# Performance work log

Measured on AMD Instinct MI355X. Metric: run time of the kernel, lower is better.

## Reference

```python
import jax, jax.numpy as jnp
import numpy as np

N = 100000   # num_nodes
E = 1600000  # num_edges (avg degree 16)
IN = 128     # input_dim
H = 4        # num_heads
D = 32       # hidden_dim per head (H*D == 128)
NEG_SLOPE = 0.2


def setup_inputs() -> dict:
    key = jax.random.key(0)
    ks = jax.random.split(key, 8)
    s = 0.1
    x = jax.random.normal(ks[0], (N, IN), jnp.float32)
    edge_index = jax.random.randint(ks[1], (2, E), 0, N, dtype=jnp.int32)
    W_gat = jax.random.normal(ks[2], (H * D, IN), jnp.float32) * s   # GATConv lin weight
    att_src = jax.random.normal(ks[3], (H, D), jnp.float32) * s
    att_dst = jax.random.normal(ks[4], (H, D), jnp.float32) * s
    bias_gat = jnp.zeros((H * D,), jnp.float32)
    W_lin = jax.random.normal(ks[5], (IN, H * D), jnp.float32) * s   # nn.Linear weight
    b_lin = jnp.zeros((IN,), jnp.float32)
    return {"x": x, "edge_index": edge_index, "W_gat": W_gat,
            "att_src": att_src, "att_dst": att_dst, "bias_gat": bias_gat,
            "W_lin": W_lin, "b_lin": b_lin}


def reference(x, edge_index, W_gat, att_src, att_dst, bias_gat, W_lin, b_lin):
    # (eval mode: all dropouts are identity; sparse edge weights unused in original)
    h = (x @ W_gat.T).reshape(N, H, D)                 # [N,H,D] per-head projections
    a_s = jnp.einsum('nhd,hd->nh', h, att_src)         # [N,H]
    a_d = jnp.einsum('nhd,hd->nh', h, att_dst)         # [N,H]
    # add self loops (PyG default)
    loop = jnp.arange(N, dtype=edge_index.dtype)
    src = jnp.concatenate([edge_index[0], loop])       # [E+N]
    dst = jnp.concatenate([edge_index[1], loop])       # [E+N]
    logits = jax.nn.leaky_relu(a_s[src] + a_d[dst], NEG_SLOPE)  # [E+N,H]
    # segment softmax over edges grouped by destination node
    m = jax.ops.segment_max(logits, dst, num_segments=N)        # [N,H]
    e = jnp.exp(logits - m[dst])
    denom = jax.ops.segment_sum(e, dst, num_segments=N)         # [N,H]
    alpha = e / denom[dst]                                      # [E+N,H]
    # scatter-aggregate weighted source features
    agg = jax.ops.segment_sum(alpha[:, :, None] * h[src], dst, num_segments=N)
    out = agg.reshape(N, H * D) + bias_gat             # concat heads + bias
    out = jax.nn.relu(out)
    return out @ W_lin.T + b_lin                       # [N, IN]
```

## Files before the change

### kernel.cpp

```cpp
#include <hip/hip_runtime.h>
#include <hip/hip_bf16.h>
#include <hip/hip_fp16.h>

#define NN 100000
#define EE 1600000
#define INF_DIM 128
#define NHEAD 4
#define HDIM 32
#define NEG_SLOPE 0.2f

typedef __attribute__((ext_vector_type(8))) short short8;
typedef __attribute__((ext_vector_type(4))) float floatx4;

__device__ __forceinline__ unsigned short f2bf(float x) {
  union { float f; unsigned int u; } c;
  c.f = x;
  const unsigned int r = c.u + 0x7fffu + ((c.u >> 16) & 1u);
  return (unsigned short)(r >> 16);
}
__device__ __forceinline__ unsigned int cvtpk_bf16(float lo, float hi) {
  unsigned int r;
  asm("v_cvt_pk_bf16_f32 %0, %1, %2" : "=v"(r) : "v"(lo), "v"(hi));
  return r;
}
__device__ __forceinline__ unsigned int packh2(float a, float b) {
  const __half ha = __float2half(a), hb = __float2half(b);
  const unsigned short ua = *(const unsigned short*)&ha;
  const unsigned short ub = *(const unsigned short*)&hb;
  return (unsigned int)ua | ((unsigned int)ub << 16);
}
__device__ __forceinline__ float pickw(const int4 e, const int head) {
  const unsigned int d = (head & 2) ? (unsigned int)e.z : (unsigned int)e.y;
  const unsigned short us =
      (head & 1) ? (unsigned short)(d >> 16) : (unsigned short)(d & 0xffffu);
  const __half h = *(const __half*)&us;
  return __half2float(h);
}
__device__ __forceinline__ void accum8h(const uint4 g, const float c,
                                        float* acc) {
  union { uint4 u; __half2 h[4]; } v;
  v.u = g;
#pragma unroll
  for (int j = 0; j < 4; ++j) {
    const float2 f = __half22float2(v.h[j]);
    acc[2 * j] = fmaf(c, f.x, acc[2 * j]);
    acc[2 * j + 1] = fmaf(c, f.y, acc[2 * j + 1]);
  }
}

#define LDA 136

__global__ __launch_bounds__(256) void gemm_mfma(
    const float* __restrict__ Af, const unsigned short* __restrict__ Ab,
    const unsigned short* __restrict__ W16, const float* __restrict__ bias,
    unsigned short* __restrict__ Ch, float* __restrict__ Cf,
    const float* __restrict__ att_src, const float* __restrict__ att_dst,
    float* __restrict__ a_s, float* __restrict__ a_d, int M) {
  __shared__ unsigned short sA[64 * LDA];
  __shared__ unsigned short sW[128 * LDA];
  const int tid = threadIdx.x;
  const int m0 = blockIdx.x * 64;

  {
    const int r = tid >> 1;
    const int c0 = (tid & 1) * 64;
#pragma unroll
    for (int j = 0; j < 8; ++j) {
      *(uint4*)&sW[r * LDA + c0 + j * 8] =
          *(const uint4*)&W16[r * 128 + c0 + j * 8];
    }
  }
  {
    const int r = tid >> 2;
    const int gm = m0 + r;
    const int c0 = (tid & 3) * 32;
    if (gm < M) {
      if (Af) {
#pragma unroll
        for (int j = 0; j < 8; ++j) {
          const float4 v = *(const float4*)&Af[(size_t)gm * 128 + c0 + j * 4];
          uint2 u;
          u.x = cvtpk_bf16(v.x, v.y);
          u.y = cvtpk_bf16(v.z, v.w);
          *(uint2*)&sA[r * LDA + c0 + j * 4] = u;
        }
      } else {
#pragma unroll
        for (int j = 0; j < 4; ++j) {
          const uint4 v = *(const uint4*)&Ab[(size_t)gm * 128 + c0 + j * 8];
          *(uint4*)&sA[r * LDA + c0 + j * 8] = v;
        }
      }
    } else {
#pragma unroll
      for (int j = 0; j < 4; ++j) {
        uint4 z;
        z.x = z.y = z.z = z.w = 0u;
        *(uint4*)&sA[r * LDA + c0 + j * 8] = z;
      }
    }
  }
  __syncthreads();

  const int wv = tid >> 6;
  const int lane = tid & 63;
  const int l16 = lane & 15;
  const int quad = lane >> 4;

  floatx4 acc[8];
#pragma unroll
  for (int i = 0; i < 8; ++i) acc[i] = (floatx4){0.f, 0.f, 0.f, 0.f};

  const unsigned short* aRow = &sA[(wv * 16 + l16) * LDA + quad * 8];
#pragma unroll
  for (int kc = 0; kc < 4; ++kc) {
    const short8 afrag = *(const short8*)(aRow + kc * 32);
#pragma unroll
    for (int nt = 0; nt < 8; ++nt) {
      const short8 bfrag =
          *(const short8*)&sW[(nt * 16 + l16) * LDA + kc * 32 + quad * 8];
      acc[nt] =
          __builtin_amdgcn_mfma_f32_16x16x32_bf16(afrag, bfrag, acc[nt], 0, 0, 0);
    }
  }

  const int mrow = m0 + wv * 16 + quad * 4;
#pragma unroll
  for (int nt = 0; nt < 8; ++nt) {
    const int col = nt * 16 + l16;
    const float bv = Cf ? bias[col] : 0.f;
#pragma unroll
    for (int r = 0; r < 4; ++r) {
      const int gm = mrow + r;
      if (gm < M) {
        const float v = acc[nt][r];
        if (Ch) {
          const __half hh = __float2half(v);
          Ch[(size_t)gm * 128 + col] = *(const unsigned short*)&hh;
        } else {
          Cf[(size_t)gm * 128 + col] = v + bv;
        }
      }
    }
  }

  if (a_s) {
    float avs[8], avd[8];
#pragma unroll
    for (int nt = 0; nt < 8; ++nt) {
      avs[nt] = att_src[nt * 16 + l16];
      avd[nt] = att_dst[nt * 16 + l16];
    }
#pragma unroll
    for (int r = 0; r < 4; ++r) {
      float ps0 = acc[0][r] * avs[0] + acc[1][r] * avs[1];
      float ps1 = acc[2][r] * avs[2] + acc[3][r] * avs[3];
      float ps2 = acc[4][r] * avs[4] + acc[5][r] * avs[5];
      float ps3 = acc[6][r] * avs[6] + acc[7][r] * avs[7];
      float pd0 = acc[0][r] * avd[0] + acc[1][r] * avd[1];
      float pd1 = acc[2][r] * avd[2] + acc[3][r] * avd[3];
      float pd2 = acc[4][r] * avd[4] + acc[5][r] * avd[5];
      float pd3 = acc[6][r] * avd[6] + acc[7][r] * avd[7];
#pragma unroll
      for (int off = 1; off < 16; off <<= 1) {
        ps0 += __shfl_xor(ps0, off);
        ps1 += __shfl_xor(ps1, off);
        ps2 += __shfl_xor(ps2, off);
        ps3 += __shfl_xor(ps3, off);
        pd0 += __shfl_xor(pd0, off);
        pd1 += __shfl_xor(pd1, off);
        pd2 += __shfl_xor(pd2, off);
        pd3 += __shfl_xor(pd3, off);
      }
      const int gm = mrow + r;
      if (gm < M) {
        const int hs = l16 & 3;
        float vs = ps0;
        if (hs == 1) vs = ps1;
        if (hs == 2) vs = ps2;
        if (hs == 3) vs = ps3;
        float vd = pd0;
        if (hs == 1) vd = pd1;
        if (hs == 2) vd = pd2;
        if (hs == 3) vd = pd3;
        if (l16 < 4)
          a_s[gm * 4 + hs] = vs;
        else if (l16 < 8)
          a_d[gm * 4 + hs] = vd;
      }
    }
  }
}

__global__ void hist_kernel(const int* __restrict__ dst, int* __restrict__ deg,
                            const float* __restrict__ Wg,
                            const float* __restrict__ Wl,
                            unsigned short* __restrict__ Wg16,
                            unsigned short* __restrict__ Wl16) {
  const int i = blockIdx.x * blockDim.x + threadIdx.x;
  if (i < 8192) {
    const int m = i >> 12;
    const int j = i & 4095;
    const float4 v = m ? ((const float4*)Wl)[j] : ((const float4*)Wg)[j];
    ushort4 u;
    u.x = f2bf(v.x);
    u.y = f2bf(v.y);
    u.z = f2bf(v.z);
    u.w = f2bf(v.w);
    if (m)
      ((ushort4*)Wl16)[j] = u;
    else
      ((ushort4*)Wg16)[j] = u;
  }
  if (i < EE) atomicAdd(&deg[dst[i]], 1);
}

__global__ __launch_bounds__(256) void alloc_kernel(const int* __restrict__ deg,
                                                    int* __restrict__ rowptr,
                                                    int* __restrict__ cur,
                                                    int* __restrict__ counter) {
  const int i = blockIdx.x * blockDim.x + threadIdx.x;
  const int lane = threadIdx.x & 63;
  const int d = (i < NN) ? deg[i] : 0;
  int s = d;
#pragma unroll
  for (int off = 1; off < 64; off <<= 1) {
    const int v = __shfl_up(s, off, 64);
    if (lane >= off) s += v;
  }
  const int total = __shfl(s, 63, 64);
  int base = 0;
  if (lane == 63) base = atomicAdd(counter, total);
  base = __shfl(base, 63, 64);
  const int p = base + s - d;
  if (i < NN) {
    rowptr[i] = p;
    cur[i] = p;
  }
}

__global__ void scatter_kernel(const int* __restrict__ src,
                               const int* __restrict__ dst,
                               const float* __restrict__ a_s,
                               const float* __restrict__ a_d,
                               int* __restrict__ cur, int4* __restrict__ ebuf) {
  const int iA = blockIdx.x * blockDim.x + threadIdx.x;
  const int iB = iA + (EE / 2);
  const int sA_ = src[iA];
  const int dA = dst[iA];
  const int sB_ = src[iB];
  const int dB = dst[iB];
  const int pA = atomicAdd(&cur[dA], 1);
  const int pB = atomicAdd(&cur[dB], 1);
  const float4 asA = *(const float4*)&a_s[sA_ * 4];
  const float4 adA = *(const float4*)&a_d[dA * 4];
  const float4 asB = *(const float4*)&a_s[sB_ * 4];
  const float4 adB = *(const float4*)&a_d[dB * 4];
  float4 lA, lB;
  lA.x = asA.x + adA.x;
  lA.y = asA.y + adA.y;
  lA.z = asA.z + adA.z;
  lA.w = asA.w + adA.w;
  lB.x = asB.x + adB.x;
  lB.y = asB.y + adB.y;
  lB.z = asB.z + adB.z;
  lB.w = asB.w + adB.w;
  lA.x = lA.x > 0.f ? lA.x : NEG_SLOPE * lA.x;
  lA.y = lA.y > 0.f ? lA.y : NEG_SLOPE * lA.y;
  lA.z = lA.z > 0.f ? lA.z : NEG_SLOPE * lA.z;
  lA.w = lA.w > 0.f ? lA.w : NEG_SLOPE * lA.w;
  lB.x = lB.x > 0.f ? lB.x : NEG_SLOPE * lB.x;
  lB.y = lB.y > 0.f ? lB.y : NEG_SLOPE * lB.y;
  lB.z = lB.z > 0.f ? lB.z : NEG_SLOPE * lB.z;
  lB.w = lB.w > 0.f ? lB.w : NEG_SLOPE * lB.w;
  int4 eA, eB;
  eA.x = sA_;
  eA.y = (int)packh2(__expf(lA.x), __expf(lA.y));
  eA.z = (int)packh2(__expf(lA.z), __expf(lA.w));
  eA.w = 0;
  eB.x = sB_;
  eB.y = (int)packh2(__expf(lB.x), __expf(lB.y));
  eB.z = (int)packh2(__expf(lB.z), __expf(lB.w));
  eB.w = 0;
  ebuf[pA] = eA;
  ebuf[pB] = eB;
}

__global__ __launch_bounds__(256) void aggregate_kernel(
    const uint4* __restrict__ hbd4, const float* __restrict__ a_s,
    const float* __restrict__ a_d, const float* __restrict__ bias_gat,
    const int* __restrict__ rowptr, const int* __restrict__ deg,
    const int4* __restrict__ ebuf, uint4* __restrict__ obd4) {
  const int wave = (blockIdx.x * blockDim.x + threadIdx.x) >> 6;
  if (wave >= NN) return;
  const int lane = threadIdx.x & 63;
  const int q = lane >> 4;
  const int f = lane & 15;
  const int head = f >> 2;
  const int n = wave;

  float acc[8];
  float ds;
  {
    const float l0 = a_s[n * 4 + head] + a_d[n * 4 + head];
    const float l = fmaxf(l0, NEG_SLOPE * l0);
    float cs = __expf(l);
    if (q != 0) cs = 0.f;
    union { uint4 u; __half2 h[4]; } v;
    v.u = hbd4[(size_t)n * 16 + f];
#pragma unroll
    for (int j = 0; j < 4; ++j) {
      const float2 fv = __half22float2(v.h[j]);
      acc[2 * j] = cs * fv.x;
      acc[2 * j + 1] = cs * fv.y;
    }
    ds = cs;
  }

  const int beg = rowptr[n];
  const int end = beg + deg[n];
  for (int i = beg; i < end; i += 16) {
    int4 e0, e1, e2, e3;
    {
      const int i0 = i + q, i1 = i + 4 + q, i2 = i + 8 + q, i3 = i + 12 + q;
      e0 = ebuf[i0 < end ? i0 : end - 1];
      e1 = ebuf[i1 < end ? i1 : end - 1];
      e2 = ebuf[i2 < end ? i2 : end - 1];
      e3 = ebuf[i3 < end ? i3 : end - 1];
    }
    const uint4 g0 = hbd4[(size_t)e0.x * 16 + f];
    const uint4 g1 = hbd4[(size_t)e1.x * 16 + f];
    const uint4 g2 = hbd4[(size_t)e2.x * 16 + f];
    const uint4 g3 = hbd4[(size_t)e3.x * 16 + f];
    float c0 = pickw(e0, head);
    float c1 = pickw(e1, head);
    float c2 = pickw(e2, head);
    float c3 = pickw(e3, head);
    if (i + q >= end) c0 = 0.f;
    if (i + 4 + q >= end) c1 = 0.f;
    if (i + 8 + q >= end) c2 = 0.f;
    if (i + 12 + q >= end) c3 = 0.f;
    accum8h(g0, c0, acc);
    accum8h(g1, c1, acc);
    accum8h(g2, c2, acc);
    accum8h(g3, c3, acc);
    ds += c0 + c1 + c2 + c3;
  }

#pragma unroll
  for (int j = 0; j < 8; ++j) {
    acc[j] += __shfl_xor(acc[j], 16);
    acc[j] += __shfl_xor(acc[j], 32);
  }
  ds += __shfl_xor(ds, 16);
  ds += __shfl_xor(ds, 32);

  if (q == 0) {
    const float inv = 1.0f / ds;
    const float4 b0 = *(const float4*)&bias_gat[f * 8];
    const float4 b1 = *(const float4*)&bias_gat[f * 8 + 4];
    float v0 = acc[0] * inv + b0.x;
    float v1 = acc[1] * inv + b0.y;
    float v2 = acc[2] * inv + b0.z;
    float v3 = acc[3] * inv + b0.w;
    float v4 = acc[4] * inv + b1.x;
    float v5 = acc[5] * inv + b1.y;
    float v6 = acc[6] * inv + b1.z;
    float v7 = acc[7] * inv + b1.w;
    v0 = v0 > 0.f ? v0 : 0.f;
    v1 = v1 > 0.f ? v1 : 0.f;
    v2 = v2 > 0.f ? v2 : 0.f;
    v3 = v3 > 0.f ? v3 : 0.f;
    v4 = v4 > 0.f ? v4 : 0.f;
    v5 = v5 > 0.f ? v5 : 0.f;
    v6 = v6 > 0.f ? v6 : 0.f;
    v7 = v7 > 0.f ? v7 : 0.f;
    uint4 r;
    r.x = (unsigned int)f2bf(v0) | ((unsigned int)f2bf(v1) << 16);
    r.y = (unsigned int)f2bf(v2) | ((unsigned int)f2bf(v3) << 16);
    r.z = (unsigned int)f2bf(v4) | ((unsigned int)f2bf(v5) << 16);
    r.w = (unsigned int)f2bf(v6) | ((unsigned int)f2bf(v7) << 16);
    obd4[(size_t)n * 16 + f] = r;
  }
}

extern "C" void kernel_launch(void* const* d_in, const int* in_sizes, int n_in,
                              void* d_out, int out_size, void* d_ws,
                              size_t ws_size, hipStream_t stream) {
  const float* x = (const float*)d_in[0];
  const int* ei = (const int*)d_in[1];
  const float* W_gat = (const float*)d_in[2];
  const float* att_src = (const float*)d_in[3];
  const float* att_dst = (const float*)d_in[4];
  const float* bias_gat = (const float*)d_in[5];
  const float* W_lin = (const float*)d_in[6];
  const float* b_lin = (const float*)d_in[7];
  float* out = (float*)d_out;

  char* ws = (char*)d_ws;
  size_t off = 0;
  unsigned short* hb = (unsigned short*)(ws + off);
  off += (size_t)NN * 128 * 2;
  unsigned short* ob = (unsigned short*)(ws + off);
  off += (size_t)NN * 128 * 2;
  float* a_s = (float*)(ws + off); off += (size_t)NN * 4 * 4;
  float* a_d = (float*)(ws + off); off += (size_t)NN * 4 * 4;
  int* deg = (int*)(ws + off); off += (size_t)NN * 4;
  int* rowptr = (int*)(ws + off); off += (size_t)(NN + 4) * 4;
  int* cur = (int*)(ws + off); off += (size_t)NN * 4;
  int* counter = (int*)(ws + off); off += 16;
  unsigned short* Wg16 = (unsigned short*)(ws + off); off += 128 * 128 * 2;
  unsigned short* Wl16 = (unsigned short*)(ws + off); off += 128 * 128 * 2;
  int4* ebuf = (int4*)(ws + off); off += (size_t)EE * 16;

  const int* src = ei;
  const int* dst = ei + EE;

  hipMemsetAsync(deg, 0, (size_t)NN * 4, stream);
  hipMemsetAsync(counter, 0, 16, stream);
  hist_kernel<<<(EE + 255) / 256, 256, 0, stream>>>(dst, deg, W_gat, W_lin,
                                                    Wg16, Wl16);
  alloc_kernel<<<(NN + 255) / 256, 256, 0, stream>>>(deg, rowptr, cur, counter);
  gemm_mfma<<<(NN + 63) / 64, 256, 0, stream>>>(x, nullptr, Wg16, nullptr, hb,
                                                nullptr, att_src, att_dst, a_s,
                                                a_d, NN);
  scatter_kernel<<<(EE / 2 + 255) / 256, 256, 0, stream>>>(src, dst, a_s, a_d,
                                                           cur, ebuf);
  aggregate_kernel<<<(NN + 3) / 4, 256, 0, stream>>>(
      (const uint4*)hb, a_s, a_d, bias_gat, rowptr, deg, ebuf,
      (uint4*)ob);
  gemm_mfma<<<(NN + 63) / 64, 256, 0, stream>>>(nullptr, ob, Wl16, b_lin,
                                                nullptr, out, nullptr, nullptr,
                                                nullptr, nullptr, NN);
}
```

Before: 389.4 us.

## Fuse degree histogram into persistent GEMM kernel and convert weights in-kernel

```diff
diff --git a/kernel.cpp b/kernel.cpp
--- a/kernel.cpp
+++ b/kernel.cpp
@@ -9,6 +9,8 @@
 #define HDIM 32
 #define NEG_SLOPE 0.2f
 
+#define GB 768
+
 typedef __attribute__((ext_vector_type(8))) short short8;
 typedef __attribute__((ext_vector_type(4))) float floatx4;
 
@@ -52,167 +54,172 @@
 
 __global__ __launch_bounds__(256) void gemm_mfma(
     const float* __restrict__ Af, const unsigned short* __restrict__ Ab,
-    const unsigned short* __restrict__ W16, const float* __restrict__ bias,
+    const float* __restrict__ W, const float* __restrict__ bias,
     unsigned short* __restrict__ Ch, float* __restrict__ Cf,
     const float* __restrict__ att_src, const float* __restrict__ att_dst,
-    float* __restrict__ a_s, float* __restrict__ a_d, int M) {
+    float* __restrict__ a_s, float* __restrict__ a_d,
+    const int* __restrict__ dstE, int* __restrict__ deg, int M) {
   __shared__ unsigned short sA[64 * LDA];
   __shared__ unsigned short sW[128 * LDA];
   const int tid = threadIdx.x;
-  const int m0 = blockIdx.x * 64;
+
+  if (dstE) {
+    for (int e = blockIdx.x * 256 + tid; e < EE; e += GB * 256)
+      atomicAdd(&deg[dstE[e]], 1);
+  }
 
   {
     const int r = tid >> 1;
     const int c0 = (tid & 1) * 64;
 #pragma unroll
-    for (int j = 0; j < 8; ++j) {
-      *(uint4*)&sW[r * LDA + c0 + j * 8] =
-          *(const uint4*)&W16[r * 128 + c0 + j * 8];
-    }
-  }
-  {
-    const int r = tid >> 2;
-    const int gm = m0 + r;
-    const int c0 = (tid & 3) * 32;
-    if (gm < M) {
-      if (Af) {
-#pragma unroll
-        for (int j = 0; j < 8; ++j) {
-          const float4 v = *(const float4*)&Af[(size_t)gm * 128 + c0 + j * 4];
-          uint2 u;
-          u.x = cvtpk_bf16(v.x, v.y);
-          u.y = cvtpk_bf16(v.z, v.w);
-          *(uint2*)&sA[r * LDA + c0 + j * 4] = u;
-        }
-      } else {
-#pragma unroll
-        for (int j = 0; j < 4; ++j) {
-          const uint4 v = *(const uint4*)&Ab[(size_t)gm * 128 + c0 + j * 8];
-          *(uint4*)&sA[r * LDA + c0 + j * 8] = v;
-        }
-      }
-    } else {
-#pragma unroll
-      for (int j = 0; j < 4; ++j) {
-        uint4 z;
-        z.x = z.y = z.z = z.w = 0u;
-        *(uint4*)&sA[r * LDA + c0 + j * 8] = z;
-      }
-    }
-  }
-  __syncthreads();
+    for (int j = 0; j < 16; ++j) {
+      const float4 v = *(const float4*)&W[r * 128 + c0 + j * 4];
+      uint2 u;
+      u.x = cvtpk_bf16(v.x, v.y);
+      u.y = cvtpk_bf16(v.z, v.w);
+      *(uint2*)&sW[r * LDA + c0 + j * 4] = u;
+    }
+  }
 
   const int wv = tid >> 6;
   const int lane = tid & 63;
   const int l16 = lane & 15;
   const int quad = lane >> 4;
-
-  floatx4 acc[8];
-#pragma unroll
-  for (int i = 0; i < 8; ++i) acc[i] = (floatx4){0.f, 0.f, 0.f, 0.f};
-
-  const unsigned short* aRow = &sA[(wv * 16 + l16) * LDA + quad * 8];
-#pragma unroll
-  for (int kc = 0; kc < 4; ++kc) {
-    const short8 afrag = *(const short8*)(aRow + kc * 32);
-#pragma unroll
-    for (int nt = 0; nt < 8; ++nt) {
-      const short8 bfrag =
-          *(const short8*)&sW[(nt * 16 + l16) * LDA + kc * 32 + quad * 8];
-      acc[nt] =
-          __builtin_amdgcn_mfma_f32_16x16x32_bf16(afrag, bfrag, acc[nt], 0, 0, 0);
-    }
-  }
-
-  const int mrow = m0 + wv * 16 + quad * 4;
-#pragma unroll
-  for (int nt = 0; nt < 8; ++nt) {
-    const int col = nt * 16 + l16;
-    const float bv = Cf ? bias[col] : 0.f;
-#pragma unroll
-    for (int r = 0; r < 4; ++r) {
-      const int gm = mrow + r;
-      if (gm < M) {
-        const float v = acc[nt][r];
-        if (Ch) {
-          const __half hh = __float2half(v);
-          Ch[(size_t)gm * 128 + col] = *(const unsigned short*)&hh;
-        } else {
-          Cf[(size_t)gm * 128 + col] = v + bv;
-        }
-      }
-    }
-  }
-
+  const int ntiles = (M + 63) >> 6;
+
+  float avs[8], avd[8];
   if (a_s) {
-    float avs[8], avd[8];
 #pragma unroll
     for (int nt = 0; nt < 8; ++nt) {
       avs[nt] = att_src[nt * 16 + l16];
       avd[nt] = att_dst[nt * 16 + l16];
     }
-#pragma unroll
-    for (int r = 0; r < 4; ++r) {
-      float ps0 = acc[0][r] * avs[0] + acc[1][r] * avs[1];
-      float ps1 = acc[2][r] * avs[2] + acc[3][r] * avs[3];
-      float ps2 = acc[4][r] * avs[4] + acc[5][r] * avs[5];
-      float ps3 = acc[6][r] * avs[6] + acc[7][r] * avs[7];
-      float pd0 = acc[0][r] * avd[0] + acc[1][r] * avd[1];
-      float pd1 = acc[2][r] * avd[2] + acc[3][r] * avd[3];
-      float pd2 = acc[4][r] * avd[4] + acc[5][r] * avd[5];
-      float pd3 = acc[6][r] * avd[6] + acc[7][r] * avd[7];
-#pragma unroll
-      for (int off = 1; off < 16; off <<= 1) {
-        ps0 += __shfl_xor(ps0, off);
-        ps1 += __shfl_xor(ps1, off);
-        ps2 += __shfl_xor(ps2, off);
-        ps3 += __shfl_xor(ps3, off);
-        pd0 += __shfl_xor(pd0, off);
-        pd1 += __shfl_xor(pd1, off);
-        pd2 += __shfl_xor(pd2, off);
-        pd3 += __shfl_xor(pd3, off);
+  }
+
+  for (int t = blockIdx.x; t < ntiles; t += GB) {
+    const int m0 = t * 64;
+    __syncthreads();
+    {
+      const int r = tid >> 2;
+      const int gm = m0 + r;
+      const int c0 = (tid & 3) * 32;
+      if (gm < M) {
+        if (Af) {
+#pragma unroll
+          for (int j = 0; j < 8; ++j) {
+            const float4 v = *(const float4*)&Af[(size_t)gm * 128 + c0 + j * 4];
+            uint2 u;
+            u.x = cvtpk_bf16(v.x, v.y);
+            u.y = cvtpk_bf16(v.z, v.w);
+            *(uint2*)&sA[r * LDA + c0 + j * 4] = u;
+          }
+        } else {
+#pragma unroll
+          for (int j = 0; j < 4; ++j) {
+            const uint4 v = *(const uint4*)&Ab[(size_t)gm * 128 + c0 + j * 8];
+            union { uint4 u; __half2 h[4]; } hv;
+            hv.u = v;
+            uint4 o;
+            float2 f0 = __half22float2(hv.h[0]);
+            float2 f1 = __half22float2(hv.h[1]);
+            float2 f2 = __half22float2(hv.h[2]);
+            float2 f3 = __half22float2(hv.h[3]);
+            o.x = cvtpk_bf16(f0.x, f0.y);
+            o.y = cvtpk_bf16(f1.x, f1.y);
+            o.z = cvtpk_bf16(f2.x, f2.y);
+            o.w = cvtpk_bf16(f3.x, f3.y);
+            *(uint4*)&sA[r * LDA + c0 + j * 8] = o;
+          }
+        }
+      } else {
+#pragma unroll
+        for (int j = 0; j < 4; ++j) {
+          uint4 z;
+          z.x = z.y = z.z = z.w = 0u;
+          *(uint4*)&sA[r * LDA + c0 + j * 8] = z;
+        }
       }
-      const int gm = mrow + r;
-      if (gm < M) {
-        const int hs = l16 & 3;
-        float vs = ps0;
-        if (hs == 1) vs = ps1;
-        if (hs == 2) vs = ps2;
-        if (hs == 3) vs = ps3;
-        float vd = pd0;
-        if (hs == 1) vd = pd1;
-        if (hs == 2) vd = pd2;
-        if (hs == 3) vd = pd3;
-        if (l16 < 4)
-          a_s[gm * 4 + hs] = vs;
-        else if (l16 < 8)
-          a_d[gm * 4 + hs] = vd;
+    }
+    __syncthreads();
+
+    floatx4 acc[8];
+#pragma unroll
+    for (int i = 0; i < 8; ++i) acc[i] = (floatx4){0.f, 0.f, 0.f, 0.f};
+
+    const unsigned short* aRow = &sA[(wv * 16 + l16) * LDA + quad * 8];
+#pragma unroll
+    for (int kc = 0; kc < 4; ++kc) {
+      const short8 afrag = *(const short8*)(aRow + kc * 32);
+#pragma unroll
+      for (int nt = 0; nt < 8; ++nt) {
+        const short8 bfrag =
+            *(const short8*)&sW[(nt * 16 + l16) * LDA + kc * 32 + quad * 8];
+        acc[nt] = __builtin_amdgcn_mfma_f32_16x16x32_bf16(afrag, bfrag,
+                                                          acc[nt], 0, 0, 0);
       }
     }
-  }
-}
-
-__global__ void hist_kernel(const int* __restrict__ dst, int* __restrict__ deg,
-                            const float* __restrict__ Wg,
-                            const float* __restrict__ Wl,
-                            unsigned short* __restrict__ Wg16,
-                            unsigned short* __restrict__ Wl16) {
-  const int i = blockIdx.x * blockDim.x + threadIdx.x;
-  if (i < 8192) {
-    const int m = i >> 12;
-    const int j = i & 4095;
-    const float4 v = m ? ((const float4*)Wl)[j] : ((const float4*)Wg)[j];
-    ushort4 u;
-    u.x = f2bf(v.x);
-    u.y = f2bf(v.y);
-    u.z = f2bf(v.z);
-    u.w = f2bf(v.w);
-    if (m)
-      ((ushort4*)Wl16)[j] = u;
-    else
-      ((ushort4*)Wg16)[j] = u;
-  }
-  if (i < EE) atomicAdd(&deg[dst[i]], 1);
+
+    const int mrow = m0 + wv * 16 + quad * 4;
+#pragma unroll
+    for (int nt = 0; nt < 8; ++nt) {
+      const int col = nt * 16 + l16;
+      const float bv = Cf ? bias[col] : 0.f;
+#pragma unroll
+      for (int r = 0; r < 4; ++r) {
+        const int gm = mrow + r;
+        if (gm < M) {
+          const float v = acc[nt][r];
+          if (Ch) {
+            const __half hh = __float2half(v);
+            Ch[(size_t)gm * 128 + col] = *(const unsigned short*)&hh;
+          } else {
+            Cf[(size_t)gm * 128 + col] = v + bv;
+          }
+        }
+      }
+    }
+
+    if (a_s) {
+#pragma unroll
+      for (int r = 0; r < 4; ++r) {
+        float ps0 = acc[0][r] * avs[0] + acc[1][r] * avs[1];
+        float ps1 = acc[2][r] * avs[2] + acc[3][r] * avs[3];
+        float ps2 = acc[4][r] * avs[4] + acc[5][r] * avs[5];
+        float ps3 = acc[6][r] * avs[6] + acc[7][r] * avs[7];
+        float pd0 = acc[0][r] * avd[0] + acc[1][r] * avd[1];
+        float pd1 = acc[2][r] * avd[2] + acc[3][r] * avd[3];
+        float pd2 = acc[4][r] * avd[4] + acc[5][r] * avd[5];
+        float pd3 = acc[6][r] * avd[6] + acc[7][r] * avd[7];
+#pragma unroll
+        for (int off = 1; off < 16; off <<= 1) {
+          ps0 += __shfl_xor(ps0, off);
+          ps1 += __shfl_xor(ps1, off);
+          ps2 += __shfl_xor(ps2, off);
+          ps3 += __shfl_xor(ps3, off);
+          pd0 += __shfl_xor(pd0, off);
+          pd1 += __shfl_xor(pd1, off);
+          pd2 += __shfl_xor(pd2, off);
+          pd3 += __shfl_xor(pd3, off);
+        }
+        const int gm = mrow + r;
+        if (gm < M) {
+          const int hs = l16 & 3;
+          float vs = ps0;
+          if (hs == 1) vs = ps1;
+          if (hs == 2) vs = ps2;
+          if (hs == 3) vs = ps3;
+          float vd = pd0;
+          if (hs == 1) vd = pd1;
+          if (hs == 2) vd = pd2;
+          if (hs == 3) vd = pd3;
+          if (l16 < 4)
+            a_s[gm * 4 + hs] = vs;
+          else if (l16 < 8)
+            a_d[gm * 4 + hs] = vd;
+        }
+      }
+    }
+  }
 }
 
 __global__ __launch_bounds__(256) void alloc_kernel(const int* __restrict__ deg,
@@ -376,10 +383,10 @@
     v6 = v6 > 0.f ? v6 : 0.f;
     v7 = v7 > 0.f ? v7 : 0.f;
     uint4 r;
-    r.x = (unsigned int)f2bf(v0) | ((unsigned int)f2bf(v1) << 16);
-    r.y = (unsigned int)f2bf(v2) | ((unsigned int)f2bf(v3) << 16);
-    r.z = (unsigned int)f2bf(v4) | ((unsigned int)f2bf(v5) << 16);
-    r.w = (unsigned int)f2bf(v6) | ((unsigned int)f2bf(v7) << 16);
+    r.x = packh2(v0, v1);
+    r.y = packh2(v2, v3);
+    r.z = packh2(v4, v5);
+    r.w = packh2(v6, v7);
     obd4[(size_t)n * 16 + f] = r;
   }
 }
@@ -409,8 +416,6 @@
   int* rowptr = (int*)(ws + off); off += (size_t)(NN + 4) * 4;
   int* cur = (int*)(ws + off); off += (size_t)NN * 4;
   int* counter = (int*)(ws + off); off += 16;
-  unsigned short* Wg16 = (unsigned short*)(ws + off); off += 128 * 128 * 2;
-  unsigned short* Wl16 = (unsigned short*)(ws + off); off += 128 * 128 * 2;
   int4* ebuf = (int4*)(ws + off); off += (size_t)EE * 16;
 
   const int* src = ei;
@@ -418,18 +423,15 @@
 
   hipMemsetAsync(deg, 0, (size_t)NN * 4, stream);
   hipMemsetAsync(counter, 0, 16, stream);
-  hist_kernel<<<(EE + 255) / 256, 256, 0, stream>>>(dst, deg, W_gat, W_lin,
-                                                    Wg16, Wl16);
+  gemm_mfma<<<GB, 256, 0, stream>>>(x, nullptr, W_gat, nullptr, hb, nullptr,
+                                    att_src, att_dst, a_s, a_d, dst, deg, NN);
   alloc_kernel<<<(NN + 255) / 256, 256, 0, stream>>>(deg, rowptr, cur, counter);
-  gemm_mfma<<<(NN + 63) / 64, 256, 0, stream>>>(x, nullptr, Wg16, nullptr, hb,
-                                                nullptr, att_src, att_dst, a_s,
-                                                a_d, NN);
   scatter_kernel<<<(EE / 2 + 255) / 256, 256, 0, stream>>>(src, dst, a_s, a_d,
                                                            cur, ebuf);
   aggregate_kernel<<<(NN + 3) / 4, 256, 0, stream>>>(
       (const uint4*)hb, a_s, a_d, bias_gat, rowptr, deg, ebuf,
       (uint4*)ob);
-  gemm_mfma<<<(NN + 63) / 64, 256, 0, stream>>>(nullptr, ob, Wl16, b_lin,
-                                                nullptr, out, nullptr, nullptr,
-                                                nullptr, nullptr, NN);
-}
+  gemm_mfma<<<GB, 256, 0, stream>>>(nullptr, ob, W_lin, b_lin, nullptr, out,
+                                    nullptr, nullptr, nullptr, nullptr,
+                                    nullptr, nullptr, NN);
+}
```

Result: no change. 382.2 us (-1.8%).
